# Optimization experiments

Measured on AMD Instinct MI355X. Metric: run time of the kernel, lower is better.

Reference implementation:

```python
import jax, jax.numpy as jnp
import numpy as np

SEQ, BATCH, C_P, C, C_I = 192, 2, 128, 32, 128


def setup_inputs() -> dict:
    key = jax.random.key(0)
    ks = jax.random.split(key, 9)
    s = lambda k, shape, scale: jax.random.normal(k, shape, dtype=jnp.float32) * scale
    return {
        "p": s(ks[0], (SEQ, BATCH, C_P), 1.0),
        "gamma": jnp.ones((C_P,), jnp.float32) + s(ks[1], (C_P,), 0.02),
        "beta": s(ks[2], (C_P,), 0.02),
        "W1": s(ks[3], (C, C_P), 1.0 / np.sqrt(C_P)),
        "b1": s(ks[4], (C,), 0.02),
        "W2": s(ks[5], (C, C_P), 1.0 / np.sqrt(C_P)),
        "b2": s(ks[6], (C,), 0.02),
        "Wout": s(ks[7], (C_I, C * C), 1.0 / np.sqrt(C * C)),
        "bout": s(ks[8], (C_I,), 0.02),
    }


def reference(p, gamma, beta, W1, b1, W2, b2, Wout, bout):
    eps = 1e-5
    B = p.shape[-2]  # Batch = p.size(-2)
    # LayerNorm over c_p
    mu = jnp.mean(p, axis=-1, keepdims=True)
    var = jnp.var(p, axis=-1, keepdims=True)
    pn = (p - mu) * jax.lax.rsqrt(var + eps) * gamma + beta
    # dual linear projections, then permute (seq, batch, c) -> (batch, seq, c)
    p1 = jnp.einsum('sbp,cp->bsc', pn, W1) + b1
    p2 = jnp.einsum('sbp,cp->bsc', pn, W2) + b2
    # outer product + flatten(c,d) + linear_out, reassociated as a single contraction:
    # out[b,k,i,j] = sum_{c,d} p1[b,i,c] * p2[b,j,d] * Wout[k, c*C+d]
    Wk = Wout.reshape(Wout.shape[0], p1.shape[-1], p2.shape[-1])  # (c_i, c, c)
    out = jnp.einsum('bic,bjd,kcd->bkij', p1, p2, Wk)
    out = (out + bout[None, :, None, None]) / B  # bias is also divided, as in source
    return out  # (batch, c_i, seq, seq)
```

## Files before the change

kernel.cpp:

```cpp
#include <hip/hip_runtime.h>
#include <hip/hip_bf16.h>


#define SEQ 192
#define BATCH 2
#define CP 128
#define CDIM 32
#define CI 128

typedef __attribute__((ext_vector_type(8))) short bf16x8;
typedef __attribute__((ext_vector_type(4))) float f32x4;

static __device__ __forceinline__ short f2bf(float f) {
    unsigned u = __builtin_bit_cast(unsigned, f);
    u += 0x7fffu + ((u >> 16) & 1u);
    return (short)(u >> 16);
}

__global__ __launch_bounds__(128) void opm_pre(
    const float* __restrict__ p, const float* __restrict__ gamma,
    const float* __restrict__ beta, const float* __restrict__ W1,
    const float* __restrict__ b1, const float* __restrict__ W2,
    const float* __restrict__ b2,
    short* __restrict__ p1ws, short* __restrict__ p2ws)
{
    int row = blockIdx.x;
    int s = row >> 1, b = row & 1;
    int t = threadIdx.x;

    __shared__ float pns[CP];
    __shared__ float red[4];
    __shared__ float part[CP];

    float x = p[s * (BATCH * CP) + b * CP + t];
    float s1 = x, s2 = x * x;
    #pragma unroll
    for (int off = 32; off; off >>= 1) {
        s1 += __shfl_down(s1, off);
        s2 += __shfl_down(s2, off);
    }
    int wave = t >> 6, lane = t & 63;
    if (lane == 0) { red[wave * 2] = s1; red[wave * 2 + 1] = s2; }
    __syncthreads();
    float tot  = red[0] + red[2];
    float tot2 = red[1] + red[3];
    float mu  = tot * (1.0f / CP);
    float var = tot2 * (1.0f / CP) - mu * mu;
    float rs  = rsqrtf(var + 1e-5f);
    pns[t] = (x - mu) * rs * gamma[t] + beta[t];
    __syncthreads();

    int c = t & 63, half = t >> 6;
    const float* wrow = (c < CDIM ? W1 + c * CP : W2 + (c - CDIM) * CP) + half * 64;
    const float4* pn4 = (const float4*)(pns + half * 64);
    const float4* w4p = (const float4*)wrow;
    float acc = 0.0f;
    #pragma unroll
    for (int i = 0; i < 16; ++i) {
        float4 w4 = w4p[i];
        float4 pn = pn4[i];
        acc += w4.x * pn.x + w4.y * pn.y + w4.z * pn.z + w4.w * pn.w;
    }
    part[t] = acc;
    __syncthreads();
    if (t < 64) {
        float d = part[t] + part[t + 64];
        if (c < CDIM) {
            p1ws[(b * SEQ + s) * CDIM + c] = f2bf(d + b1[c]);
        } else {
            p2ws[(b * SEQ + s) * CDIM + (c - CDIM)] =
                f2bf(0.5f * (d + b2[c - CDIM]));
        }
    }
}

#define T2PAD 40

__global__ __launch_bounds__(256) void opm_main(
    const short* __restrict__ p1ws,
    const short* __restrict__ p2ws,
    const float* __restrict__ Wout,
    const float* __restrict__ bout,
    float* __restrict__ out)
{
    int blk = blockIdx.x;
    int b = blk >> 7, k = blk & 127;
    int tid  = threadIdx.x;
    int wave = tid >> 6, lane = tid & 63;
    int l15  = lane & 15, quad = lane >> 4;

    __shared__ short t2s[SEQ * T2PAD];

    const float* wk = Wout + k * (CDIM * CDIM);
    #pragma unroll
    for (int mi = 0; mi < 3; ++mi) {
        int j0 = (wave + mi * 4) * 16;
        bf16x8 afrag = *(const bf16x8*)(p2ws + (b * SEQ + j0 + l15) * CDIM + quad * 8);
        #pragma unroll
        for (int ni = 0; ni < 2; ++ni) {
            int c0 = ni * 16;
            const float* wrow = wk + (c0 + l15) * CDIM + quad * 8;
            bf16x8 bfrag;
            #pragma unroll
            for (int e = 0; e < 8; ++e) bfrag[e] = f2bf(wrow[e]);
            f32x4 acc = {0.0f, 0.0f, 0.0f, 0.0f};
            acc = __builtin_amdgcn_mfma_f32_16x16x32_bf16(afrag, bfrag, acc, 0, 0, 0);
            #pragma unroll
            for (int r = 0; r < 4; ++r)
                t2s[(j0 + quad * 4 + r) * T2PAD + c0 + l15] = f2bf(acc[r]);
        }
    }
    __syncthreads();

    float biask = 0.5f * bout[k];
    const short* p1b = p1ws + b * SEQ * CDIM;
    #pragma unroll
    for (int ii = 0; ii < 3; ++ii) {
        int i0 = (wave * 3 + ii) * 16;
        bf16x8 afrag = *(const bf16x8*)(p1b + (i0 + l15) * CDIM + quad * 8);
        #pragma unroll
        for (int jt = 0; jt < 12; ++jt) {
            int j0 = jt * 16;
            bf16x8 bfrag = *(const bf16x8*)(t2s + (j0 + l15) * T2PAD + quad * 8);
            f32x4 acc = {biask, biask, biask, biask};
            acc = __builtin_amdgcn_mfma_f32_16x16x32_bf16(afrag, bfrag, acc, 0, 0, 0);
            float* o = out + ((blk * SEQ) + i0 + quad * 4) * SEQ + j0 + l15;
            #pragma unroll
            for (int r = 0; r < 4; ++r)
                o[r * SEQ] = acc[r];
        }
    }
}

extern "C" void kernel_launch(void* const* d_in, const int* in_sizes, int n_in,
                              void* d_out, int out_size, void* d_ws, size_t ws_size,
                              hipStream_t stream) {
    const float* p     = (const float*)d_in[0];
    const float* gamma = (const float*)d_in[1];
    const float* beta  = (const float*)d_in[2];
    const float* W1    = (const float*)d_in[3];
    const float* b1    = (const float*)d_in[4];
    const float* W2    = (const float*)d_in[5];
    const float* b2    = (const float*)d_in[6];
    const float* Wout  = (const float*)d_in[7];
    const float* bout  = (const float*)d_in[8];
    float* out = (float*)d_out;

    short* p1ws = (short*)d_ws;
    short* p2ws = p1ws + BATCH * SEQ * CDIM;

    opm_pre<<<SEQ * BATCH, 128, 0, stream>>>(p, gamma, beta, W1, b1, W2, b2,
                                             p1ws, p2ws);
    opm_main<<<BATCH * CI, 256, 0, stream>>>(p1ws, p2ws, Wout, bout, out);
}
```

Baseline: 89.71 us.

## Split output rows across four blocks and drop LDS barrier via wave-local T2 tiles

Launches four blocks per (batch, k) pair, each handling a 48-row slice of the output, which raises the grid from 256 to 1024 blocks to fill more CUs. Each wave now computes and consumes only its own 48-column slice of the intermediate T2 tile in LDS, so the __syncthreads between the two phases is removed. The Wout bf16 fragments are also hoisted out of the inner loop. The cost is that the first-stage T2 product (p2 x Wk) is recomputed redundantly in each of the four blocks.

```diff
diff --git a/kernel.cpp b/kernel.cpp
--- a/kernel.cpp
+++ b/kernel.cpp
@@ -83,8 +83,9 @@
     const float* __restrict__ bout,
     float* __restrict__ out)
 {
-    int blk = blockIdx.x;
-    int b = blk >> 7, k = blk & 127;
+    int bk = blockIdx.x >> 2;
+    int iq = blockIdx.x & 3;
+    int b = bk >> 7, k = bk & 127;
     int tid  = threadIdx.x;
     int wave = tid >> 6, lane = tid & 63;
     int l15  = lane & 15, quad = lane >> 4;
@@ -92,39 +93,41 @@
     __shared__ short t2s[SEQ * T2PAD];
 
     const float* wk = Wout + k * (CDIM * CDIM);
+    bf16x8 bfr[2];
+    #pragma unroll
+    for (int ni = 0; ni < 2; ++ni) {
+        const float* wrow = wk + (ni * 16 + l15) * CDIM + quad * 8;
+        #pragma unroll
+        for (int e = 0; e < 8; ++e) bfr[ni][e] = f2bf(wrow[e]);
+    }
     #pragma unroll
     for (int mi = 0; mi < 3; ++mi) {
-        int j0 = (wave + mi * 4) * 16;
+        int j0 = (wave * 3 + mi) * 16;
         bf16x8 afrag = *(const bf16x8*)(p2ws + (b * SEQ + j0 + l15) * CDIM + quad * 8);
         #pragma unroll
         for (int ni = 0; ni < 2; ++ni) {
-            int c0 = ni * 16;
-            const float* wrow = wk + (c0 + l15) * CDIM + quad * 8;
-            bf16x8 bfrag;
-            #pragma unroll
-            for (int e = 0; e < 8; ++e) bfrag[e] = f2bf(wrow[e]);
             f32x4 acc = {0.0f, 0.0f, 0.0f, 0.0f};
-            acc = __builtin_amdgcn_mfma_f32_16x16x32_bf16(afrag, bfrag, acc, 0, 0, 0);
+            acc = __builtin_amdgcn_mfma_f32_16x16x32_bf16(afrag, bfr[ni], acc, 0, 0, 0);
             #pragma unroll
             for (int r = 0; r < 4; ++r)
-                t2s[(j0 + quad * 4 + r) * T2PAD + c0 + l15] = f2bf(acc[r]);
+                t2s[(j0 + quad * 4 + r) * T2PAD + ni * 16 + l15] = f2bf(acc[r]);
         }
     }
-    __syncthreads();
 
     float biask = 0.5f * bout[k];
     const short* p1b = p1ws + b * SEQ * CDIM;
+    float* obase = out + (size_t)bk * (SEQ * SEQ);
     #pragma unroll
     for (int ii = 0; ii < 3; ++ii) {
-        int i0 = (wave * 3 + ii) * 16;
+        int i0 = iq * 48 + ii * 16;
         bf16x8 afrag = *(const bf16x8*)(p1b + (i0 + l15) * CDIM + quad * 8);
         #pragma unroll
-        for (int jt = 0; jt < 12; ++jt) {
-            int j0 = jt * 16;
+        for (int jj = 0; jj < 3; ++jj) {
+            int j0 = (wave * 3 + jj) * 16;
             bf16x8 bfrag = *(const bf16x8*)(t2s + (j0 + l15) * T2PAD + quad * 8);
             f32x4 acc = {biask, biask, biask, biask};
             acc = __builtin_amdgcn_mfma_f32_16x16x32_bf16(afrag, bfrag, acc, 0, 0, 0);
-            float* o = out + ((blk * SEQ) + i0 + quad * 4) * SEQ + j0 + l15;
+            float* o = obase + (i0 + quad * 4) * SEQ + j0 + l15;
             #pragma unroll
             for (int r = 0; r < 4; ++r)
                 o[r * SEQ] = acc[r];
@@ -151,5 +154,5 @@
 
     opm_pre<<<SEQ * BATCH, 128, 0, stream>>>(p, gamma, beta, W1, b1, W2, b2,
                                              p1ws, p2ws);
-    opm_main<<<BATCH * CI, 256, 0, stream>>>(p1ws, p2ws, Wout, bout, out);
+    opm_main<<<BATCH * CI * 4, 256, 0, stream>>>(p1ws, p2ws, Wout, bout, out);
 }
```

New measurement: 88.78 us. No clear change (-1.0%).
